# Performance work log

Hardware: AMD Instinct MI355X
Metric: run time of the kernel (lower is better)

Reference implementation:

```python
import jax, jax.numpy as jnp
import numpy as np

N_NODES = 100000


def _gcn_conv(x, src, dst, W, b):
    # symmetric normalization D^{-1/2} (A+I) D^{-1/2}, self loops already in src/dst
    deg = jax.ops.segment_sum(jnp.ones_like(src, dtype=x.dtype), dst, num_segments=N_NODES)
    dinv = jnp.where(deg > 0, jax.lax.rsqrt(jnp.maximum(deg, 1e-12)), 0.0)
    norm = dinv[src] * dinv[dst]                      # [E+N]
    h = x @ W                                          # [N, out] dense GEMM first (fewer features to move)
    msg = h[src] * norm[:, None]                       # gather + scale, [E+N, out]
    out = jax.ops.segment_sum(msg, dst, num_segments=N_NODES)
    return out + b


def setup_inputs() -> dict:
    key = jax.random.key(0)
    k_x, k_e, k_w1, k_w2 = jax.random.split(key, 4)
    in_f, hid, n_cls = 512, 128, 32
    E = 1600000
    x = jax.random.normal(k_x, (N_NODES, in_f), dtype=jnp.float32)
    edge_index = jax.random.randint(k_e, (2, E), 0, N_NODES, dtype=jnp.int32)
    # Glorot-ish init for weights
    W1 = jax.random.normal(k_w1, (in_f, hid), dtype=jnp.float32) * (1.0 / np.sqrt(in_f))
    b1 = jnp.zeros((hid,), dtype=jnp.float32)
    W2 = jax.random.normal(k_w2, (hid, n_cls), dtype=jnp.float32) * (1.0 / np.sqrt(hid))
    b2 = jnp.zeros((n_cls,), dtype=jnp.float32)
    return {"x": x, "edge_index": edge_index, "W1": W1, "b1": b1, "W2": W2, "b2": b2}


def reference(x, edge_index, W1, b1, W2, b2):
    loops = jnp.arange(N_NODES, dtype=edge_index.dtype)
    src = jnp.concatenate([edge_index[0], loops])
    dst = jnp.concatenate([edge_index[1], loops])
    h = _gcn_conv(x, src, dst, W1, b1)
    h = jax.nn.relu(h)
    # dropout in eval mode (identity) for deterministic reference
    out = _gcn_conv(h, src, dst, W2, b2)
    return out
```

## Files before the change

### kernel.cpp

```cpp
#include <hip/hip_runtime.h>
#include <hip/hip_bf16.h>
#include <cstddef>


#define IN_F 512
#define HID 128
#define NCLS 32

typedef __attribute__((ext_vector_type(8))) short bf16x8;
typedef __attribute__((ext_vector_type(4))) float f32x4;

__device__ __forceinline__ unsigned short f2bf(float f) {
    union { float f; unsigned u; } v; v.f = f;
    unsigned r = v.u + 0x7fff + ((v.u >> 16) & 1);
    return (unsigned short)(r >> 16);
}
__device__ __forceinline__ float bf2f(unsigned short h) {
    union { unsigned u; float f; } v; v.u = ((unsigned)h) << 16;
    return v.f;
}
__device__ __forceinline__ float lo16(unsigned u) { return bf2f((unsigned short)(u & 0xffff)); }
__device__ __forceinline__ float hi16(unsigned u) { return bf2f((unsigned short)(u >> 16)); }

__global__ void k_histprep(const int* __restrict__ dst, int* __restrict__ deg,
                           int* __restrict__ rank, int E,
                           const float* __restrict__ W1, unsigned short* __restrict__ W1T, int PB) {
    int b = blockIdx.x;
    if (b < PB) {
        int i = b * 256 + threadIdx.x;
        int n = i >> 9, k = i & 511;
        W1T[(size_t)n * IN_F + k] = f2bf(W1[(size_t)k * HID + n]);
    } else {
        int e = (b - PB) * 256 + threadIdx.x;
        if (e < E) rank[e] = atomicAdd(&deg[dst[e]], 1);
    }
}

__global__ void k_dinv(const int* __restrict__ deg, float* __restrict__ dinv, int n,
                       unsigned* __restrict__ hsu, unsigned* __restrict__ h2su) {
    int i = blockIdx.x * 256 + threadIdx.x;
    if (i < n) dinv[i] = rsqrtf((float)deg[i] + 1.0f);
    if (blockIdx.x == 0) {
        if (threadIdx.x < 64) hsu[(size_t)n * 64 + threadIdx.x] = 0u;
        if (threadIdx.x < 16) h2su[(size_t)n * 16 + threadIdx.x] = 0u;
    }
}

__global__ __launch_bounds__(256) void k_scan1(const int* __restrict__ deg, int* __restrict__ rs,
                                               int* __restrict__ bsum, int n) {
    __shared__ int sd[256];
    int base = blockIdx.x * 2048 + threadIdx.x * 8;
    int v[8];
    int t = 0;
#pragma unroll
    for (int i = 0; i < 8; ++i) {
        int x = (base + i < n) ? ((deg[base + i] + 7) & ~7) : 0;
        v[i] = t;
        t += x;
    }
    sd[threadIdx.x] = t;
    __syncthreads();
    for (int off = 1; off < 256; off <<= 1) {
        int x = 0;
        if ((int)threadIdx.x >= off) x = sd[threadIdx.x - off];
        __syncthreads();
        if ((int)threadIdx.x >= off) sd[threadIdx.x] += x;
        __syncthreads();
    }
    int texcl = sd[threadIdx.x] - t;
#pragma unroll
    for (int i = 0; i < 8; ++i)
        if (base + i < n) rs[base + i] = texcl + v[i];
    if (threadIdx.x == 255) bsum[blockIdx.x] = sd[255];
}

__global__ void k_scan2(int* bsum, int nb) {
    if (threadIdx.x == 0 && blockIdx.x == 0) {
        int run = 0;
        for (int b = 0; b < nb; ++b) { int t = bsum[b]; bsum[b] = run; run += t; }
    }
}

__global__ void k_scan3(int* __restrict__ rs, const int* __restrict__ bsum,
                        const int* __restrict__ deg, int* __restrict__ csr, int n) {
    int i = blockIdx.x * 256 + threadIdx.x;
    if (i < n) {
        int r = rs[i] + bsum[i >> 11];
        rs[i] = r;
        int d = deg[i];
        int pc = (d + 7) & ~7;
        for (int j = d; j < pc; ++j) csr[r + j] = n;
    }
}

#define LSTR 40
#define SCHUNK 1024
__global__ __launch_bounds__(256) void k_fused(const float* __restrict__ A,
                                               const unsigned short* __restrict__ BT,
                                               const float* __restrict__ dinv,
                                               unsigned short* __restrict__ C, int M,
                                               const int* __restrict__ src, const int* __restrict__ dst,
                                               const int* __restrict__ rank, const int* __restrict__ rs,
                                               int* __restrict__ csr, int E) {
    const int bid = blockIdx.x;
    const int tid = threadIdx.x;
    if (bid & 1) {
        int base = (bid >> 1) * SCHUNK + tid;
        int d[4], s[4], rk[4];
        bool val[4];
#pragma unroll
        for (int j = 0; j < 4; ++j) {
            int e = base + j * 256;
            val[j] = e < E;
            if (val[j]) { d[j] = dst[e]; s[j] = src[e]; rk[j] = rank[e]; }
        }
#pragma unroll
        for (int j = 0; j < 4; ++j)
            if (val[j]) csr[rs[d[j]] + rk[j]] = s[j];
        return;
    }
    __shared__ unsigned short As[64 * LSTR];
    __shared__ unsigned short Bs[128 * LSTR];
    const int wave = tid >> 6;
    const int lane = tid & 63;
    const int l16 = lane & 15;
    const int q = lane >> 4;
    const int rowBase = (bid >> 1) * 64;

    const int ar = tid >> 2, akc = tid & 3;
    const int agr = rowBase + ar;
    const int bn0 = tid >> 2, bn1 = 64 + (tid >> 2), bkc = tid & 3;

    f32x4 acc[8];
#pragma unroll
    for (int nt = 0; nt < 8; ++nt) acc[nt] = (f32x4){0.f, 0.f, 0.f, 0.f};

    float4 pa0, pa1;
    uint4 pb0, pb1;
    auto load_tile = [&](int k0, float4& a0, float4& a1, uint4& b0, uint4& b1) {
        if (agr < M) {
            const float* ap = A + (size_t)agr * IN_F + k0 + akc * 8;
            a0 = *(const float4*)ap;
            a1 = *(const float4*)(ap + 4);
        } else {
            a0 = make_float4(0.f, 0.f, 0.f, 0.f);
            a1 = a0;
        }
        b0 = *(const uint4*)(BT + (size_t)bn0 * IN_F + k0 + bkc * 8);
        b1 = *(const uint4*)(BT + (size_t)bn1 * IN_F + k0 + bkc * 8);
    };

    load_tile(0, pa0, pa1, pb0, pb1);

    for (int t = 0; t < 16; ++t) {
        ushort4 lohalf, hihalf;
        lohalf.x = f2bf(pa0.x); lohalf.y = f2bf(pa0.y); lohalf.z = f2bf(pa0.z); lohalf.w = f2bf(pa0.w);
        hihalf.x = f2bf(pa1.x); hihalf.y = f2bf(pa1.y); hihalf.z = f2bf(pa1.z); hihalf.w = f2bf(pa1.w);
        *(ushort4*)(As + ar * LSTR + akc * 8) = lohalf;
        *(ushort4*)(As + ar * LSTR + akc * 8 + 4) = hihalf;
        *(uint4*)(Bs + bn0 * LSTR + bkc * 8) = pb0;
        *(uint4*)(Bs + bn1 * LSTR + bkc * 8) = pb1;
        __syncthreads();

        float4 na0, na1;
        uint4 nb0, nb1;
        if (t < 15) load_tile((t + 1) * 32, na0, na1, nb0, nb1);

        bf16x8 a_frag = *(const bf16x8*)(As + (wave * 16 + l16) * LSTR + q * 8);
        bf16x8 b_frag[8];
#pragma unroll
        for (int nt = 0; nt < 8; ++nt)
            b_frag[nt] = *(const bf16x8*)(Bs + (nt * 16 + l16) * LSTR + q * 8);
#pragma unroll
        for (int nt = 0; nt < 8; ++nt)
            acc[nt] = __builtin_amdgcn_mfma_f32_16x16x32_bf16(a_frag, b_frag[nt], acc[nt], 0, 0, 0);
        __syncthreads();
        pa0 = na0; pa1 = na1; pb0 = nb0; pb1 = nb1;
    }

#pragma unroll
    for (int r = 0; r < 4; ++r) {
        int row = rowBase + wave * 16 + q * 4 + r;
        if (row < M) {
            float sc = dinv[row];
#pragma unroll
            for (int nt = 0; nt < 8; ++nt)
                C[(size_t)row * HID + nt * 16 + l16] = f2bf(acc[nt][r] * sc);
        }
    }
}

__global__ __launch_bounds__(256) void k_agg1(const unsigned short* __restrict__ hs,
                                              const int* __restrict__ csr,
                                              const int* __restrict__ rs, const int* __restrict__ cnt,
                                              const float* __restrict__ dinv, const float* __restrict__ b1,
                                              unsigned short* __restrict__ h1, int N) {
    int v = blockIdx.x * 4 + (threadIdx.x >> 6);
    if (v >= N) return;
    int lane = threadIdx.x & 63;
    float dv = dinv[v];
    const unsigned* hrow = (const unsigned*)hs;
    unsigned u = hrow[(size_t)v * 64 + lane];
    float ax = lo16(u), ay = hi16(u);
    int start = rs[v];
    int pc = (cnt[v] + 7) & ~7;
    for (int i = 0; i < pc; i += 8) {
        int s[8];
        unsigned uu[8];
#pragma unroll
        for (int j = 0; j < 8; ++j) s[j] = csr[start + i + j];
#pragma unroll
        for (int j = 0; j < 8; ++j) uu[j] = hrow[(size_t)s[j] * 64 + lane];
#pragma unroll
        for (int j = 0; j < 8; ++j) { ax += lo16(uu[j]); ay += hi16(uu[j]); }
    }
    float2 bb = ((const float2*)b1)[lane];
    float ox = fmaxf(dv * ax + bb.x, 0.f);
    float oy = fmaxf(dv * ay + bb.y, 0.f);
    ((unsigned*)h1)[(size_t)v * 64 + lane] =
        (unsigned)f2bf(ox) | ((unsigned)f2bf(oy) << 16);
}

__global__ __launch_bounds__(256) void k_gemm2(const unsigned short* __restrict__ A,
                                               const float* __restrict__ B,
                                               const float* __restrict__ dinv,
                                               unsigned short* __restrict__ C, int M) {
    __shared__ float Bs[HID][NCLS];
    __shared__ float As[64][HID];
    const int tid = threadIdx.x;
#pragma unroll
    for (int it = 0; it < 16; ++it) {
        int idx = tid + 256 * it;
        Bs[idx >> 5][idx & 31] = B[idx];
    }
    int rowBase = blockIdx.x * 64;
    const unsigned* A2 = (const unsigned*)A;
#pragma unroll
    for (int it = 0; it < 16; ++it) {
        int idx = tid + 256 * it;
        int r = idx >> 6, c2 = idx & 63;
        int gr = rowBase + r;
        unsigned u = (gr < M) ? A2[(size_t)gr * 64 + c2] : 0u;
        As[r][2 * c2]     = lo16(u);
        As[r][2 * c2 + 1] = hi16(u);
    }
    __syncthreads();
    int col = tid & 31;
    int rg = tid >> 5;
    float acc[8];
#pragma unroll
    for (int i = 0; i < 8; ++i) acc[i] = 0.f;
    for (int k = 0; k < HID; ++k) {
        float b = Bs[k][col];
#pragma unroll
        for (int i = 0; i < 8; ++i) acc[i] += As[rg * 8 + i][k] * b;
    }
#pragma unroll
    for (int i = 0; i < 8; ++i) {
        int gr = rowBase + rg * 8 + i;
        if (gr < M) C[(size_t)gr * NCLS + col] = f2bf(acc[i] * dinv[gr]);
    }
}

__global__ __launch_bounds__(256) void k_agg2(const unsigned short* __restrict__ h2s,
                                              const int* __restrict__ csr,
                                              const int* __restrict__ rs, const int* __restrict__ cnt,
                                              const float* __restrict__ dinv, const float* __restrict__ b2,
                                              float* __restrict__ out, int N) {
    int g = threadIdx.x >> 4;
    int l = threadIdx.x & 15;
    int v = blockIdx.x * 16 + g;
    if (v >= N) return;
    float dv = dinv[v];
    const unsigned* rows = (const unsigned*)h2s;
    unsigned u = rows[(size_t)v * 16 + l];
    float ax = lo16(u), ay = hi16(u);
    int start = rs[v];
    int pc = (cnt[v] + 7) & ~7;
    for (int i = 0; i < pc; i += 8) {
        int s[8];
        unsigned uu[8];
#pragma unroll
        for (int j = 0; j < 8; ++j) s[j] = csr[start + i + j];
#pragma unroll
        for (int j = 0; j < 8; ++j) uu[j] = rows[(size_t)s[j] * 16 + l];
#pragma unroll
        for (int j = 0; j < 8; ++j) { ax += lo16(uu[j]); ay += hi16(uu[j]); }
    }
    float2 bb = ((const float2*)b2)[l];
    float2 o;
    o.x = dv * ax + bb.x;
    o.y = dv * ay + bb.y;
    *((float2*)(out + (size_t)v * NCLS) + l) = o;
}

extern "C" void kernel_launch(void* const* d_in, const int* in_sizes, int n_in,
                              void* d_out, int out_size, void* d_ws, size_t ws_size,
                              hipStream_t stream) {
    const float* x = (const float*)d_in[0];
    const int* edge_index = (const int*)d_in[1];
    const float* W1 = (const float*)d_in[2];
    const float* b1 = (const float*)d_in[3];
    const float* W2 = (const float*)d_in[4];
    const float* b2 = (const float*)d_in[5];
    float* out = (float*)d_out;

    const int N = in_sizes[0] / IN_F;
    const int E = in_sizes[1] / 2;
    const int* e_src = edge_index;
    const int* e_dst = edge_index + E;

    char* ws = (char*)d_ws;
    size_t off = 0;
    auto alloc = [&](size_t bytes) -> char* {
        char* p = ws + off;
        off += (bytes + 255) & ~(size_t)255;
        return p;
    };
    int* deg             = (int*)alloc((size_t)N * 4);
    float* dinv          = (float*)alloc((size_t)N * 4);
    int* rs              = (int*)alloc((size_t)N * 4);
    int* bsum            = (int*)alloc(1024 * 4);
    int* csr             = (int*)alloc(((size_t)E + 8 * (size_t)N) * 4);
    unsigned short* W1T  = (unsigned short*)alloc((size_t)HID * IN_F * 2);
    unsigned short* hs   = (unsigned short*)alloc((size_t)(N + 1) * HID * 2);
    unsigned short* h1   = (unsigned short*)alloc((size_t)N * HID * 2);
    unsigned short* h2s  = (unsigned short*)alloc((size_t)(N + 1) * NCLS * 2);
    int* rank            = (int*)h1;

    const int nbE = (E + 255) / 256;
    const int nbN = (N + 255) / 256;
    const int nbScan = (N + 2047) / 2048;
    const int PB = (HID * IN_F) / 256;
    const int NBG = (N + 63) / 64;

    hipMemsetAsync(deg, 0, (size_t)N * 4, stream);
    k_histprep<<<PB + nbE, 256, 0, stream>>>(e_dst, deg, rank, E, W1, W1T, PB);
    k_dinv<<<nbN, 256, 0, stream>>>(deg, dinv, N, (unsigned*)hs, (unsigned*)h2s);
    k_scan1<<<nbScan, 256, 0, stream>>>(deg, rs, bsum, N);
    k_scan2<<<1, 64, 0, stream>>>(bsum, nbScan);
    k_scan3<<<nbN, 256, 0, stream>>>(rs, bsum, deg, csr, N);

    k_fused<<<2 * NBG, 256, 0, stream>>>(x, W1T, dinv, hs, N, e_src, e_dst, rank, rs, csr, E);

    k_agg1<<<(N + 3) / 4, 256, 0, stream>>>(hs, csr, rs, deg, dinv, b1, h1, N);
    k_gemm2<<<(N + 63) / 64, 256, 0, stream>>>(h1, W2, dinv, h2s, N);
    k_agg2<<<(N + 15) / 16, 256, 0, stream>>>(h2s, csr, rs, deg, dinv, b2, out, N);
}
```

Baseline: 550.1 us.

## Overlap degree histogram with GEMM1 and defer dinv scaling to CSR-fill pass

The degree-counting atomics now run in the same launch as the first GEMM, with odd blocks doing the histogram and even blocks doing the matmul, so that pass overlaps the matmul. The dinv computation moves into the scan kernel. The GEMM output is written unscaled and rescaled by dinv in a second combined kernel that also fills the CSR. The memset and dinv kernel are replaced by one init kernel. This cuts launches and hides the atomic pass, but adds an extra read-modify-write of the bf16 hidden matrix and a second bf16 rounding step.

```diff
diff --git a/kernel.cpp b/kernel.cpp
--- a/kernel.cpp
+++ b/kernel.cpp
@@ -21,102 +21,53 @@
 }
 __device__ __forceinline__ float lo16(unsigned u) { return bf2f((unsigned short)(u & 0xffff)); }
 __device__ __forceinline__ float hi16(unsigned u) { return bf2f((unsigned short)(u >> 16)); }
-
-__global__ void k_histprep(const int* __restrict__ dst, int* __restrict__ deg,
-                           int* __restrict__ rank, int E,
-                           const float* __restrict__ W1, unsigned short* __restrict__ W1T, int PB) {
+__device__ __forceinline__ unsigned sc2(unsigned u, float s) {
+    return (unsigned)f2bf(lo16(u) * s) | ((unsigned)f2bf(hi16(u) * s) << 16);
+}
+
+__global__ void k_init(int* __restrict__ deg, int N,
+                       const float* __restrict__ W1, unsigned short* __restrict__ W1T,
+                       unsigned* __restrict__ hsu, unsigned* __restrict__ h2su, int ZB) {
     int b = blockIdx.x;
-    if (b < PB) {
-        int i = b * 256 + threadIdx.x;
+    if (b < ZB) {
+        int idx = b * 256 + threadIdx.x;
+        if (idx * 4 < N) {
+            int4 z = make_int4(0, 0, 0, 0);
+            if (idx * 4 + 3 < N) *(int4*)(deg + idx * 4) = z;
+            else for (int j = idx * 4; j < N; ++j) deg[j] = 0;
+        }
+    } else if (b < ZB + 256) {
+        int i = (b - ZB) * 256 + threadIdx.x;
         int n = i >> 9, k = i & 511;
         W1T[(size_t)n * IN_F + k] = f2bf(W1[(size_t)k * HID + n]);
     } else {
-        int e = (b - PB) * 256 + threadIdx.x;
-        if (e < E) rank[e] = atomicAdd(&deg[dst[e]], 1);
-    }
-}
-
-__global__ void k_dinv(const int* __restrict__ deg, float* __restrict__ dinv, int n,
-                       unsigned* __restrict__ hsu, unsigned* __restrict__ h2su) {
-    int i = blockIdx.x * 256 + threadIdx.x;
-    if (i < n) dinv[i] = rsqrtf((float)deg[i] + 1.0f);
-    if (blockIdx.x == 0) {
-        if (threadIdx.x < 64) hsu[(size_t)n * 64 + threadIdx.x] = 0u;
-        if (threadIdx.x < 16) h2su[(size_t)n * 16 + threadIdx.x] = 0u;
-    }
-}
-
-__global__ __launch_bounds__(256) void k_scan1(const int* __restrict__ deg, int* __restrict__ rs,
-                                               int* __restrict__ bsum, int n) {
-    __shared__ int sd[256];
-    int base = blockIdx.x * 2048 + threadIdx.x * 8;
-    int v[8];
-    int t = 0;
-#pragma unroll
-    for (int i = 0; i < 8; ++i) {
-        int x = (base + i < n) ? ((deg[base + i] + 7) & ~7) : 0;
-        v[i] = t;
-        t += x;
-    }
-    sd[threadIdx.x] = t;
-    __syncthreads();
-    for (int off = 1; off < 256; off <<= 1) {
-        int x = 0;
-        if ((int)threadIdx.x >= off) x = sd[threadIdx.x - off];
-        __syncthreads();
-        if ((int)threadIdx.x >= off) sd[threadIdx.x] += x;
-        __syncthreads();
-    }
-    int texcl = sd[threadIdx.x] - t;
-#pragma unroll
-    for (int i = 0; i < 8; ++i)
-        if (base + i < n) rs[base + i] = texcl + v[i];
-    if (threadIdx.x == 255) bsum[blockIdx.x] = sd[255];
-}
-
-__global__ void k_scan2(int* bsum, int nb) {
-    if (threadIdx.x == 0 && blockIdx.x == 0) {
-        int run = 0;
-        for (int b = 0; b < nb; ++b) { int t = bsum[b]; bsum[b] = run; run += t; }
-    }
-}
-
-__global__ void k_scan3(int* __restrict__ rs, const int* __restrict__ bsum,
-                        const int* __restrict__ deg, int* __restrict__ csr, int n) {
-    int i = blockIdx.x * 256 + threadIdx.x;
-    if (i < n) {
-        int r = rs[i] + bsum[i >> 11];
-        rs[i] = r;
-        int d = deg[i];
-        int pc = (d + 7) & ~7;
-        for (int j = d; j < pc; ++j) csr[r + j] = n;
+        if (threadIdx.x < 64) hsu[(size_t)N * 64 + threadIdx.x] = 0u;
+        if (threadIdx.x < 16) h2su[(size_t)N * 16 + threadIdx.x] = 0u;
     }
 }
 
 #define LSTR 40
 #define SCHUNK 1024
-__global__ __launch_bounds__(256) void k_fused(const float* __restrict__ A,
+__global__ __launch_bounds__(256) void k_mega1(const float* __restrict__ A,
                                                const unsigned short* __restrict__ BT,
-                                               const float* __restrict__ dinv,
                                                unsigned short* __restrict__ C, int M,
-                                               const int* __restrict__ src, const int* __restrict__ dst,
-                                               const int* __restrict__ rank, const int* __restrict__ rs,
-                                               int* __restrict__ csr, int E) {
+                                               const int* __restrict__ dst,
+                                               int* __restrict__ deg, int* __restrict__ rank, int E) {
     const int bid = blockIdx.x;
     const int tid = threadIdx.x;
     if (bid & 1) {
         int base = (bid >> 1) * SCHUNK + tid;
-        int d[4], s[4], rk[4];
+        int d[4];
         bool val[4];
 #pragma unroll
         for (int j = 0; j < 4; ++j) {
             int e = base + j * 256;
             val[j] = e < E;
-            if (val[j]) { d[j] = dst[e]; s[j] = src[e]; rk[j] = rank[e]; }
+            if (val[j]) d[j] = dst[e];
         }
 #pragma unroll
         for (int j = 0; j < 4; ++j)
-            if (val[j]) csr[rs[d[j]] + rk[j]] = s[j];
+            if (val[j]) rank[base + j * 256] = atomicAdd(&deg[d[j]], 1);
         return;
     }
     __shared__ unsigned short As[64 * LSTR];
@@ -182,11 +133,94 @@
     for (int r = 0; r < 4; ++r) {
         int row = rowBase + wave * 16 + q * 4 + r;
         if (row < M) {
-            float sc = dinv[row];
 #pragma unroll
             for (int nt = 0; nt < 8; ++nt)
-                C[(size_t)row * HID + nt * 16 + l16] = f2bf(acc[nt][r] * sc);
-        }
+                C[(size_t)row * HID + nt * 16 + l16] = f2bf(acc[nt][r]);
+        }
+    }
+}
+
+__global__ __launch_bounds__(256) void k_scan1(const int* __restrict__ deg, int* __restrict__ rs,
+                                               int* __restrict__ bsum, float* __restrict__ dinv, int n) {
+    __shared__ int sd[256];
+    int base = blockIdx.x * 2048 + threadIdx.x * 8;
+    int v[8];
+    int t = 0;
+#pragma unroll
+    for (int i = 0; i < 8; ++i) {
+        int d = (base + i < n) ? deg[base + i] : 0;
+        if (base + i < n) dinv[base + i] = rsqrtf((float)d + 1.0f);
+        int x = (base + i < n) ? ((d + 7) & ~7) : 0;
+        v[i] = t;
+        t += x;
+    }
+    sd[threadIdx.x] = t;
+    __syncthreads();
+    for (int off = 1; off < 256; off <<= 1) {
+        int x = 0;
+        if ((int)threadIdx.x >= off) x = sd[threadIdx.x - off];
+        __syncthreads();
+        if ((int)threadIdx.x >= off) sd[threadIdx.x] += x;
+        __syncthreads();
+    }
+    int texcl = sd[threadIdx.x] - t;
+#pragma unroll
+    for (int i = 0; i < 8; ++i)
+        if (base + i < n) rs[base + i] = texcl + v[i];
+    if (threadIdx.x == 255) bsum[blockIdx.x] = sd[255];
+}
+
+__global__ void k_scan2(int* bsum, int nb) {
+    if (threadIdx.x == 0 && blockIdx.x == 0) {
+        int run = 0;
+        for (int b = 0; b < nb; ++b) { int t = bsum[b]; bsum[b] = run; run += t; }
+    }
+}
+
+__global__ void k_scan3(int* __restrict__ rs, const int* __restrict__ bsum,
+                        const int* __restrict__ deg, int* __restrict__ csr, int n) {
+    int i = blockIdx.x * 256 + threadIdx.x;
+    if (i < n) {
+        int r = rs[i] + bsum[i >> 11];
+        rs[i] = r;
+        int d = deg[i];
+        int pc = (d + 7) & ~7;
+        for (int j = d; j < pc; ++j) csr[r + j] = n;
+    }
+}
+
+__global__ __launch_bounds__(256) void k_mega2(const int* __restrict__ src, const int* __restrict__ dst,
+                                               const int* __restrict__ rank, const int* __restrict__ rs,
+                                               int* __restrict__ csr, int E,
+                                               unsigned* __restrict__ hu, const float* __restrict__ dinv,
+                                               int N) {
+    const int bid = blockIdx.x;
+    const int tid = threadIdx.x;
+    if (bid & 1) {
+        int base = (bid >> 1) * SCHUNK + tid;
+        int d[4], s[4], rk[4];
+        bool val[4];
+#pragma unroll
+        for (int j = 0; j < 4; ++j) {
+            int e = base + j * 256;
+            val[j] = e < E;
+            if (val[j]) { d[j] = dst[e]; s[j] = src[e]; rk[j] = rank[e]; }
+        }
+#pragma unroll
+        for (int j = 0; j < 4; ++j)
+            if (val[j]) csr[rs[d[j]] + rk[j]] = s[j];
+        return;
+    }
+    int row = (bid >> 1) * 64 + (tid >> 2);
+    if (row >= N) return;
+    float dv = dinv[row];
+    uint4* p = (uint4*)(hu + (size_t)row * 64) + (tid & 3) * 4;
+#pragma unroll
+    for (int j = 0; j < 4; ++j) {
+        uint4 u = p[j];
+        u.x = sc2(u.x, dv); u.y = sc2(u.y, dv);
+        u.z = sc2(u.z, dv); u.w = sc2(u.w, dv);
+        p[j] = u;
     }
 }
 
@@ -328,20 +362,17 @@
     unsigned short* h2s  = (unsigned short*)alloc((size_t)(N + 1) * NCLS * 2);
     int* rank            = (int*)h1;
 
-    const int nbE = (E + 255) / 256;
     const int nbN = (N + 255) / 256;
     const int nbScan = (N + 2047) / 2048;
-    const int PB = (HID * IN_F) / 256;
+    const int ZB = (N / 4 + 255) / 256;
     const int NBG = (N + 63) / 64;
 
-    hipMemsetAsync(deg, 0, (size_t)N * 4, stream);
-    k_histprep<<<PB + nbE, 256, 0, stream>>>(e_dst, deg, rank, E, W1, W1T, PB);
-    k_dinv<<<nbN, 256, 0, stream>>>(deg, dinv, N, (unsigned*)hs, (unsigned*)h2s);
-    k_scan1<<<nbScan, 256, 0, stream>>>(deg, rs, bsum, N);
+    k_init<<<ZB + 256 + 1, 256, 0, stream>>>(deg, N, W1, W1T, (unsigned*)hs, (unsigned*)h2s, ZB);
+    k_mega1<<<2 * NBG, 256, 0, stream>>>(x, W1T, hs, N, e_dst, deg, rank, E);
+    k_scan1<<<nbScan, 256, 0, stream>>>(deg, rs, bsum, dinv, N);
     k_scan2<<<1, 64, 0, stream>>>(bsum, nbScan);
     k_scan3<<<nbN, 256, 0, stream>>>(rs, bsum, deg, csr, N);
-
-    k_fused<<<2 * NBG, 256, 0, stream>>>(x, W1T, dinv, hs, N, e_src, e_dst, rank, rs, csr, E);
+    k_mega2<<<2 * NBG, 256, 0, stream>>>(e_src, e_dst, rank, rs, csr, E, (unsigned*)hs, dinv, N);
 
     k_agg1<<<(N + 3) / 4, 256, 0, stream>>>(hs, csr, rs, deg, dinv, b1, h1, N);
     k_gemm2<<<(N + 63) / 64, 256, 0, stream>>>(h1, W2, dinv, h2s, N);
```

Result: no change. 551.9 us (+0.3%).
